# Kernel optimization log

Measured on AMD Instinct MI355X. Metric: run time of the kernel, lower is better.

## Reference

```python
import jax, jax.numpy as jnp
import numpy as np

NUM_VIEW = 300
NUM_ANGLE = 12
NUM_DEPTH = 4
GRASP_MAX_WIDTH = 0.1
B, C, NS, NG = 2, 512, 2048, 2000


def generate_grasp_views(N=NUM_VIEW):
    phi = (np.sqrt(5.0) - 1.0) / 2.0  # fibonacci sphere
    idxs = jnp.arange(N, dtype=jnp.float32)
    Z = (2.0 * idxs + 1.0) / N - 1.0
    r = jnp.sqrt(jnp.maximum(1.0 - Z * Z, 0.0))
    X = r * jnp.cos(2.0 * jnp.pi * idxs * phi)
    Y = r * jnp.sin(2.0 * jnp.pi * idxs * phi)
    return jnp.stack([X, Y, Z], -1)  # [N,3]


def viewpoint_params_to_matrix(towards, angle):
    # towards [...,3], angle [...]
    ax = towards
    zero = jnp.zeros_like(ax[..., 0])
    ay = jnp.stack([-ax[..., 1], ax[..., 0], zero], -1)
    ynorm = jnp.linalg.norm(ay, axis=-1, keepdims=True)
    ay = jnp.where(ynorm == 0, jnp.array([0.0, 1.0, 0.0], ax.dtype), ay)
    ax = ax / jnp.linalg.norm(ax, axis=-1, keepdims=True)
    ay = ay / jnp.linalg.norm(ay, axis=-1, keepdims=True)
    az = jnp.cross(ax, ay)
    c, s = jnp.cos(angle), jnp.sin(angle)
    one = jnp.ones_like(c)
    R1 = jnp.stack([one, zero * 0 + jnp.zeros_like(c), jnp.zeros_like(c),
                    jnp.zeros_like(c), c, -s,
                    jnp.zeros_like(c), s, c], -1).reshape(angle.shape + (3, 3))
    R2 = jnp.stack([ax, ay, az], -1)  # axes as columns
    return R2 @ R1


def conv1d(x, w, b):
    # 1x1 Conv1d == channel matmul. x [B,Ci,N], w [Co,Ci]
    return jnp.einsum('oi,bin->bon', w, x) + b[None, :, None]


def knn1(q, ref):
    # K=1 nearest neighbor indices of q [Nq,3] in ref [Nr,3]
    d = (jnp.sum(q * q, -1, keepdims=True) + jnp.sum(ref * ref, -1)[None, :]
         - 2.0 * q @ ref.T)
    return jnp.argmin(d, axis=-1)


def normalize_tensor(t, eps=1e-8):
    mx = jnp.max(t, -1, keepdims=True)
    mn = jnp.min(t, -1, keepdims=True)
    return (t - mn) / (mx - mn + eps)


def _process_one(seed_xyz, pose, gpoints, gscores, gwidths, views, views_rot):
    R, t = pose[:, :3], pose[:, 3]
    gp_trans = gpoints @ R.T + t                      # [Ng,3]
    gv_trans = views @ R.T                            # [V,3]
    gv_rot_trans = jnp.einsum('ij,vjk->vik', R, views_rot)  # [V,3,3]
    view_inds = knn1(views, gv_trans)                 # [V]
    gv_rot_trans = gv_rot_trans[view_inds]            # [V,3,3]
    nn_inds = knn1(seed_xyz, gp_trans)                # [Ns]
    gp_out = gp_trans[nn_inds]                        # [Ns,3]
    # gather seed dim first (Ns<Ng) then reindex views; axes independent
    sc = gscores[nn_inds][:, view_inds]               # [Ns,V,A,D]
    wd = gwidths[nn_inds][:, view_inds]
    rot = jnp.broadcast_to(gv_rot_trans[None], (seed_xyz.shape[0],) + gv_rot_trans.shape)
    return gp_out, rot, sc, wd


def setup_inputs() -> dict:
    key = jax.random.key(0)
    ks = jax.random.split(key, 16)
    seed_features = jax.random.normal(ks[0], (B, C, NS), jnp.float32)
    point_clouds = jax.random.normal(ks[1], (B, NS, 3), jnp.float32) * 0.2
    Rq = np.linalg.qr(np.asarray(jax.random.normal(ks[2], (B, 3, 3))))[0].astype(np.float32)
    trans = jax.random.normal(ks[3], (B, 3, 1), jnp.float32) * 0.1
    object_pose = jnp.concatenate([jnp.asarray(Rq), trans], -1)  # [B,3,4]
    grasp_points = jax.random.normal(ks[4], (B, NG, 3), jnp.float32) * 0.2
    grasp_labels = jax.random.uniform(ks[5], (B, NG, NUM_VIEW, NUM_ANGLE, NUM_DEPTH)) * 1.2 - 0.2
    grasp_offsets = jax.random.uniform(ks[6], (B, NG, NUM_VIEW, NUM_ANGLE, NUM_DEPTH)) * 0.15
    w = lambda k, co, ci: jax.random.normal(k, (co, ci), jnp.float32) * 0.05
    bz = lambda co: jnp.zeros((co,), jnp.float32)
    return {
        'seed_features': seed_features, 'point_clouds': point_clouds,
        'object_pose': object_pose, 'grasp_points': grasp_points,
        'grasp_labels': grasp_labels, 'grasp_offsets': grasp_offsets,
        'aw1_w': w(ks[7], C, C), 'aw1_b': bz(C),
        'aw2_w': w(ks[8], C, C), 'aw2_b': bz(C),
        'aw3_w': w(ks[9], NUM_VIEW, C), 'aw3_b': bz(NUM_VIEW),
        'sw1_w': w(ks[10], C, C), 'sw1_b': bz(C),
        'sw2_w': w(ks[11], NUM_DEPTH * NUM_ANGLE * 2, C), 'sw2_b': bz(NUM_DEPTH * NUM_ANGLE * 2),
    }


def reference(seed_features, point_clouds, object_pose, grasp_points,
              grasp_labels, grasp_offsets, aw1_w, aw1_b, aw2_w, aw2_b,
              aw3_w, aw3_b, sw1_w, sw1_b, sw2_w, sw2_b):
    Bx, Cx, Ns = seed_features.shape
    # --- ApproachNet (eval branch) ---
    res = jax.nn.relu(conv1d(seed_features, aw1_w, aw1_b))
    res = jax.nn.relu(conv1d(res, aw2_w, aw2_b))
    view_scores = conv1d(res, aw3_w, aw3_b).transpose(0, 2, 1)  # [B,Ns,V]
    top_view_inds = jnp.argmax(view_scores, -1)                 # [B,Ns]
    views = generate_grasp_views(NUM_VIEW)
    vp_xyz = views[top_view_inds]                               # [B,Ns,3]
    vp_rot = viewpoint_params_to_matrix(-vp_xyz, jnp.zeros(vp_xyz.shape[:-1], vp_xyz.dtype))
    # --- SWADNet ---
    f = jax.nn.relu(conv1d(res, sw1_w, sw1_b))
    f = conv1d(f, sw2_w, sw2_b)
    f = f.reshape(Bx, 2, NUM_ANGLE, NUM_DEPTH, Ns).transpose(0, 1, 4, 2, 3)
    grasp_score_pred = f[:, 0]   # [B,Ns,A,D]
    grasp_width_pred = f[:, 1]
    # --- process_grasp_labels (vmapped over batch) ---
    views_rot = viewpoint_params_to_matrix(-views, jnp.zeros((NUM_VIEW,), views.dtype))
    gp, rot, sc, wd = jax.vmap(_process_one, in_axes=(0, 0, 0, 0, 0, None, None))(
        point_clouds, object_pose, grasp_points, grasp_labels, grasp_offsets, views, views_rot)
    gmask = (sc <= 0.6) & (sc > 0)
    graspness = normalize_tensor(
        gmask.astype(jnp.float32).reshape(Bx, Ns, NUM_VIEW, -1).mean(-1))  # [B,Ns,V]
    label_mask = (sc > 0) & (wd <= GRASP_MAX_WIDTH)
    sc = jnp.where(label_mask, sc, 0.0)
    # --- match_grasp_view_and_label ---
    bi = jnp.arange(Bx)[:, None]
    ni = jnp.arange(Ns)[None, :]
    top_rot = rot[bi, ni, top_view_inds]  # [B,Ns,3,3]
    top_sc = sc[bi, ni, top_view_inds]    # [B,Ns,A,D]
    top_wd = wd[bi, ni, top_view_inds]
    u_max = jnp.max(top_sc)
    po = top_sc > 0
    safe = jnp.where(po, top_sc, 1.0)
    u_min = jnp.min(jnp.where(po, top_sc, jnp.inf))
    new_sc = jnp.log(u_max / safe) / (jnp.log(u_max / u_min) + 1e-8)
    top_sc = jnp.where(po, new_sc, top_sc)
    return (view_scores, vp_rot, grasp_score_pred, grasp_width_pred,
            top_rot, top_sc, top_wd, graspness, gp)
```

## Files before the change

kernel.cpp:

```cpp
#include <hip/hip_runtime.h>
#include <math.h>
#include <stdint.h>

#define NV 300
#define NA 12
#define ND 4
#define NB 2
#define NC 512
#define NSD 2048
#define NGP 2000
#define ROWLEN 14400

__global__ void __launch_bounds__(512) k_setup_all(
    const float* __restrict__ pose, float* __restrict__ views_rot_g,
    int* __restrict__ view_inds, float* __restrict__ Rsel, int* __restrict__ mmx) {
  int b = blockIdx.x, tid = threadIdx.x;
  __shared__ float sv[NV][3];
  __shared__ float svr[NV][9];
  __shared__ float R[9];
  __shared__ float gv[NV][3];
  __shared__ float gvr[NV];
  if (b == 0 && tid == 0) { mmx[0] = 0; mmx[1] = 0x7f800000; }
  if (tid < 9) R[tid] = pose[b * 12 + (tid / 3) * 4 + (tid % 3)];
  if (tid < NV) {
    float fi = (float)tid;
    float Z = (2.0f * fi + 1.0f) / 300.0f - 1.0f;
    float r = sqrtf(fmaxf(1.0f - Z * Z, 0.0f));
    float ang = (6.28318530717958647692f * fi) * 0.61803398874989484820f;
    float X = r * cosf(ang);
    float Y = r * sinf(ang);
    sv[tid][0] = X; sv[tid][1] = Y; sv[tid][2] = Z;
    float ax0 = -X, ax1 = -Y, ax2 = -Z;
    float ay0 = -ax1, ay1 = ax0, ay2 = 0.f;
    float ynorm = sqrtf(ay0 * ay0 + ay1 * ay1 + ay2 * ay2);
    if (ynorm == 0.f) { ay0 = 0.f; ay1 = 1.f; ay2 = 0.f; }
    float an = sqrtf(ax0 * ax0 + ax1 * ax1 + ax2 * ax2);
    ax0 /= an; ax1 /= an; ax2 /= an;
    float ayn = sqrtf(ay0 * ay0 + ay1 * ay1 + ay2 * ay2);
    ay0 /= ayn; ay1 /= ayn; ay2 /= ayn;
    float az0 = ax1 * ay2 - ax2 * ay1;
    float az1 = ax2 * ay0 - ax0 * ay2;
    float az2 = ax0 * ay1 - ax1 * ay0;
    svr[tid][0] = ax0; svr[tid][1] = ay0; svr[tid][2] = az0;
    svr[tid][3] = ax1; svr[tid][4] = ay1; svr[tid][5] = az1;
    svr[tid][6] = ax2; svr[tid][7] = ay2; svr[tid][8] = az2;
    if (b == 0) {
      float* m = views_rot_g + tid * 9;
#pragma unroll
      for (int i = 0; i < 9; i++) m[i] = svr[tid][i];
    }
  }
  __syncthreads();
  if (tid < NV) {
    float vx = sv[tid][0], vy = sv[tid][1], vz = sv[tid][2];
    float x = R[0] * vx + R[1] * vy + R[2] * vz;
    float y = R[3] * vx + R[4] * vy + R[5] * vz;
    float z = R[6] * vx + R[7] * vy + R[8] * vz;
    gv[tid][0] = x; gv[tid][1] = y; gv[tid][2] = z;
    gvr[tid] = x * x + y * y + z * z;
  }
  __syncthreads();
  if (tid < NV) {
    float qx = sv[tid][0], qy = sv[tid][1], qz = sv[tid][2];
    float qq = qx * qx + qy * qy + qz * qz;
    float best = INFINITY; int bi = 0;
    for (int u = 0; u < NV; u++) {
      float dot = qx * gv[u][0] + qy * gv[u][1] + qz * gv[u][2];
      float d = qq + gvr[u] - 2.f * dot;
      if (d < best) { best = d; bi = u; }
    }
    view_inds[b * NV + tid] = bi;
    const float* vr = svr[bi];
    float* o = Rsel + (b * NV + tid) * 9;
    for (int i = 0; i < 3; i++)
      for (int j = 0; j < 3; j++)
        o[i * 3 + j] = R[i * 3 + 0] * vr[0 + j] + R[i * 3 + 1] * vr[3 + j] + R[i * 3 + 2] * vr[6 + j];
  }
}

__global__ void __launch_bounds__(256) k_nn(
    const float* __restrict__ pc, const float* __restrict__ pose,
    const float* __restrict__ gpoints, int* __restrict__ nn_inds,
    float* __restrict__ out_gp) {
  int b = blockIdx.y;
  int s0 = blockIdx.x * 32;
  int tid = threadIdx.x;
  __shared__ float4 pts[NGP];
  __shared__ float P[12];
  if (tid < 12) P[tid] = pose[b * 12 + tid];
  __syncthreads();
  for (int i = tid; i < NGP; i += 256) {
    float px = gpoints[((size_t)b * NGP + i) * 3 + 0];
    float py = gpoints[((size_t)b * NGP + i) * 3 + 1];
    float pz = gpoints[((size_t)b * NGP + i) * 3 + 2];
    float x = P[0] * px + P[1] * py + P[2] * pz + P[3];
    float y = P[4] * px + P[5] * py + P[6] * pz + P[7];
    float z = P[8] * px + P[9] * py + P[10] * pz + P[11];
    pts[i] = make_float4(x, y, z, x * x + y * y + z * z);
  }
  __syncthreads();
  int sl = tid & 31, chunk = tid >> 5;
  int s = s0 + sl;
  float qx = pc[((size_t)b * NSD + s) * 3 + 0];
  float qy = pc[((size_t)b * NSD + s) * 3 + 1];
  float qz = pc[((size_t)b * NSD + s) * 3 + 2];
  float qq = qx * qx + qy * qy + qz * qz;
  int i0 = chunk * 250;
  float best = INFINITY; int bi = i0;
  for (int i = i0; i < i0 + 250; i++) {
    float4 p = pts[i];
    float d = qq + p.w - 2.f * (qx * p.x + qy * p.y + qz * p.z);
    if (d < best) { best = d; bi = i; }
  }
  __shared__ float rb[8][33];
  __shared__ int ri[8][33];
  rb[chunk][sl] = best; ri[chunk][sl] = bi;
  __syncthreads();
  if (tid < 32) {
    float bb = INFINITY; int ii = 0;
    for (int c = 0; c < 8; c++) {
      float v = rb[c][tid];
      if (v < bb) { bb = v; ii = ri[c][tid]; }
    }
    nn_inds[b * NSD + s0 + tid] = ii;
    float4 p = pts[ii];
    out_gp[((size_t)b * NSD + s0 + tid) * 3 + 0] = p.x;
    out_gp[((size_t)b * NSD + s0 + tid) * 3 + 1] = p.y;
    out_gp[((size_t)b * NSD + s0 + tid) * 3 + 2] = p.z;
  }
}

template <bool RELU, bool GUARD_M>
__global__ void __launch_bounds__(256) gemm128(
    const float* __restrict__ W, const float* __restrict__ X,
    const float* __restrict__ bias, float* __restrict__ Y,
    int O, int Cin, int N) {
  int b = blockIdx.z;
  const float* Xb = X + (size_t)b * Cin * N;
  float* Yb = Y + (size_t)b * O * N;
  int m0 = blockIdx.y * 128, n0 = blockIdx.x * 64;
  __shared__ float As[16][132];
  __shared__ float Bs[16][64];
  int tid = threadIdx.x;
  int mW = tid >> 1;
  int kW = (tid & 1) * 8;
  int kX = tid >> 4, nX = (tid & 15) * 4;
  int ty = tid >> 4, tx = tid & 15;
  bool okm = !GUARD_M || (m0 + mW) < O;
  float4 a0, a1, bv;
  {
    const float* wp = &W[(size_t)(m0 + mW) * Cin + kW];
    a0 = okm ? *(const float4*)wp : make_float4(0.f, 0.f, 0.f, 0.f);
    a1 = okm ? *(const float4*)(wp + 4) : make_float4(0.f, 0.f, 0.f, 0.f);
    bv = *(const float4*)&Xb[(size_t)kX * N + n0 + nX];
  }
  float acc[8][4] = {};
  for (int k0 = 0; k0 < Cin; k0 += 16) {
    __syncthreads();
    As[kW + 0][mW] = a0.x; As[kW + 1][mW] = a0.y;
    As[kW + 2][mW] = a0.z; As[kW + 3][mW] = a0.w;
    As[kW + 4][mW] = a1.x; As[kW + 5][mW] = a1.y;
    As[kW + 6][mW] = a1.z; As[kW + 7][mW] = a1.w;
    *(float4*)&Bs[kX][nX] = bv;
    __syncthreads();
    if (k0 + 16 < Cin) {
      const float* wp = &W[(size_t)(m0 + mW) * Cin + k0 + 16 + kW];
      a0 = okm ? *(const float4*)wp : make_float4(0.f, 0.f, 0.f, 0.f);
      a1 = okm ? *(const float4*)(wp + 4) : make_float4(0.f, 0.f, 0.f, 0.f);
      bv = *(const float4*)&Xb[(size_t)(k0 + 16 + kX) * N + n0 + nX];
    }
#pragma unroll
    for (int kk = 0; kk < 16; kk++) {
      float4 x0 = *(const float4*)&As[kk][ty * 8];
      float4 x1 = *(const float4*)&As[kk][ty * 8 + 4];
      float4 y = *(const float4*)&Bs[kk][tx * 4];
      acc[0][0] = fmaf(x0.x, y.x, acc[0][0]); acc[0][1] = fmaf(x0.x, y.y, acc[0][1]);
      acc[0][2] = fmaf(x0.x, y.z, acc[0][2]); acc[0][3] = fmaf(x0.x, y.w, acc[0][3]);
      acc[1][0] = fmaf(x0.y, y.x, acc[1][0]); acc[1][1] = fmaf(x0.y, y.y, acc[1][1]);
      acc[1][2] = fmaf(x0.y, y.z, acc[1][2]); acc[1][3] = fmaf(x0.y, y.w, acc[1][3]);
      acc[2][0] = fmaf(x0.z, y.x, acc[2][0]); acc[2][1] = fmaf(x0.z, y.y, acc[2][1]);
      acc[2][2] = fmaf(x0.z, y.z, acc[2][2]); acc[2][3] = fmaf(x0.z, y.w, acc[2][3]);
      acc[3][0] = fmaf(x0.w, y.x, acc[3][0]); acc[3][1] = fmaf(x0.w, y.y, acc[3][1]);
      acc[3][2] = fmaf(x0.w, y.z, acc[3][2]); acc[3][3] = fmaf(x0.w, y.w, acc[3][3]);
      acc[4][0] = fmaf(x1.x, y.x, acc[4][0]); acc[4][1] = fmaf(x1.x, y.y, acc[4][1]);
      acc[4][2] = fmaf(x1.x, y.z, acc[4][2]); acc[4][3] = fmaf(x1.x, y.w, acc[4][3]);
      acc[5][0] = fmaf(x1.y, y.x, acc[5][0]); acc[5][1] = fmaf(x1.y, y.y, acc[5][1]);
      acc[5][2] = fmaf(x1.y, y.z, acc[5][2]); acc[5][3] = fmaf(x1.y, y.w, acc[5][3]);
      acc[6][0] = fmaf(x1.z, y.x, acc[6][0]); acc[6][1] = fmaf(x1.z, y.y, acc[6][1]);
      acc[6][2] = fmaf(x1.z, y.z, acc[6][2]); acc[6][3] = fmaf(x1.z, y.w, acc[6][3]);
      acc[7][0] = fmaf(x1.w, y.x, acc[7][0]); acc[7][1] = fmaf(x1.w, y.y, acc[7][1]);
      acc[7][2] = fmaf(x1.w, y.z, acc[7][2]); acc[7][3] = fmaf(x1.w, y.w, acc[7][3]);
    }
  }
#pragma unroll
  for (int i = 0; i < 8; i++) {
    int m = m0 + ty * 8 + i;
    if (GUARD_M && m >= O) break;
    float bi = bias[m];
    float4 v;
    v.x = acc[i][0] + bi; v.y = acc[i][1] + bi;
    v.z = acc[i][2] + bi; v.w = acc[i][3] + bi;
    if (RELU) {
      v.x = fmaxf(v.x, 0.f); v.y = fmaxf(v.y, 0.f);
      v.z = fmaxf(v.z, 0.f); v.w = fmaxf(v.w, 0.f);
    }
    *(float4*)&Yb[(size_t)m * N + n0 + (tx << 2)] = v;
  }
}

__global__ void __launch_bounds__(256) gemm_sw2(
    const float* __restrict__ W, const float* __restrict__ X,
    const float* __restrict__ bias, float* __restrict__ gsp,
    float* __restrict__ gwp) {
  const int O = 96, Cin = NC, N = NSD;
  int b = blockIdx.z;
  const float* Xb = X + (size_t)b * Cin * N;
  int m0 = blockIdx.y * 64, n0 = blockIdx.x * 64;
  __shared__ float As[16][68];
  __shared__ float Bs[16][64];
  int tid = threadIdx.x;
  int mW = tid >> 2, kW = (tid & 3) * 4;
  int kX = tid >> 4, nX = (tid & 15) * 4;
  int ty = tid >> 4, tx = tid & 15;
  float acc[4][4] = {};
  for (int k0 = 0; k0 < Cin; k0 += 16) {
    float4 wv;
    if ((m0 + mW) < O)
      wv = *(const float4*)&W[(size_t)(m0 + mW) * Cin + k0 + kW];
    else
      wv = make_float4(0.f, 0.f, 0.f, 0.f);
    As[kW + 0][mW] = wv.x; As[kW + 1][mW] = wv.y;
    As[kW + 2][mW] = wv.z; As[kW + 3][mW] = wv.w;
    *(float4*)&Bs[kX][nX] = *(const float4*)&Xb[(size_t)(k0 + kX) * N + n0 + nX];
    __syncthreads();
#pragma unroll
    for (int kk = 0; kk < 16; kk++) {
      float4 a = *(const float4*)&As[kk][ty << 2];
      float4 bv = *(const float4*)&Bs[kk][tx << 2];
      acc[0][0] = fmaf(a.x, bv.x, acc[0][0]); acc[0][1] = fmaf(a.x, bv.y, acc[0][1]);
      acc[0][2] = fmaf(a.x, bv.z, acc[0][2]); acc[0][3] = fmaf(a.x, bv.w, acc[0][3]);
      acc[1][0] = fmaf(a.y, bv.x, acc[1][0]); acc[1][1] = fmaf(a.y, bv.y, acc[1][1]);
      acc[1][2] = fmaf(a.y, bv.z, acc[1][2]); acc[1][3] = fmaf(a.y, bv.w, acc[1][3]);
      acc[2][0] = fmaf(a.z, bv.x, acc[2][0]); acc[2][1] = fmaf(a.z, bv.y, acc[2][1]);
      acc[2][2] = fmaf(a.z, bv.z, acc[2][2]); acc[2][3] = fmaf(a.z, bv.w, acc[2][3]);
      acc[3][0] = fmaf(a.w, bv.x, acc[3][0]); acc[3][1] = fmaf(a.w, bv.y, acc[3][1]);
      acc[3][2] = fmaf(a.w, bv.z, acc[3][2]); acc[3][3] = fmaf(a.w, bv.w, acc[3][3]);
    }
    __syncthreads();
  }
  int m = m0 + ty * 4;
  if (m < O) {
    float b0 = bias[m], b1 = bias[m + 1], b2 = bias[m + 2], b3 = bias[m + 3];
#pragma unroll
    for (int j = 0; j < 4; j++) {
      int n = n0 + (tx << 2) + j;
      float4 v;
      v.x = acc[0][j] + b0; v.y = acc[1][j] + b1;
      v.z = acc[2][j] + b2; v.w = acc[3][j] + b3;
      size_t base = ((size_t)b * NSD + n) * 48;
      if (m < 48) *(float4*)&gsp[base + m] = v;
      else        *(float4*)&gwp[base + m - 48] = v;
    }
  }
}

__global__ void __launch_bounds__(256) k_view(
    const float* __restrict__ vs_t, const float* __restrict__ views_rot,
    const float* __restrict__ Rsel, int* __restrict__ tv_inds,
    float* __restrict__ o_vs, float* __restrict__ o_vprot,
    float* __restrict__ o_trot) {
  int b = blockIdx.y, n0 = blockIdx.x * 32;
  int tx = threadIdx.x, ty = threadIdx.y;
  __shared__ float tile[32][33];
  __shared__ float bval[8][32];
  __shared__ int bidx[8][32];
  const float* src = vs_t + (size_t)b * NV * NSD;
  float best = -INFINITY; int bi = 0;
  for (int v0 = 0; v0 < NV; v0 += 32) {
    int vlim = (NV - v0 < 32) ? (NV - v0) : 32;
    for (int i = ty; i < vlim; i += 8)
      tile[i][tx] = src[(size_t)(v0 + i) * NSD + n0 + tx];
    __syncthreads();
    if (v0 + tx < NV) {
#pragma unroll
      for (int j = 0; j < 4; j++) {
        int nl = ty * 4 + j;
        o_vs[((size_t)b * NSD + n0 + nl) * NV + v0 + tx] = tile[tx][nl];
      }
    }
    for (int i = ty; i < vlim; i += 8) {
      float val = tile[i][tx];
      if (val > best) { best = val; bi = v0 + i; }
    }
    __syncthreads();
  }
  bval[ty][tx] = best; bidx[ty][tx] = bi;
  __syncthreads();
  if (ty == 0) {
    for (int t = 1; t < 8; t++) {
      float v = bval[t][tx]; int ii = bidx[t][tx];
      if (v > best || (v == best && ii < bi)) { best = v; bi = ii; }
    }
    int n = n0 + tx;
    tv_inds[b * NSD + n] = bi;
    const float* vr = views_rot + bi * 9;
    const float* rs = Rsel + (b * NV + bi) * 9;
    float* o1 = o_vprot + ((size_t)b * NSD + n) * 9;
    float* o4 = o_trot + ((size_t)b * NSD + n) * 9;
#pragma unroll
    for (int i = 0; i < 9; i++) { o1[i] = vr[i]; o4[i] = rs[i]; }
  }
}

__global__ void __launch_bounds__(256) k_grasp(
    const float* __restrict__ gscores, const float* __restrict__ goffsets,
    const int* __restrict__ nn_inds, const int* __restrict__ tv_inds,
    const int* __restrict__ view_inds, float* __restrict__ o_grsp,
    float* __restrict__ o_twd, float* __restrict__ raw) {
  int b = blockIdx.y, s = blockIdx.x, tid = threadIdx.x;
  __shared__ int vi[NV];
  for (int v = tid; v < NV; v += 256) vi[v] = view_inds[b * NV + v];
  __syncthreads();
  int nn = nn_inds[b * NSD + s];
  int tv = tv_inds[b * NSD + s];
  int vit = vi[tv];
  const float* srow = gscores + ((size_t)(b * NGP + nn)) * ROWLEN;
  const float* wrow = goffsets + ((size_t)(b * NGP + nn)) * ROWLEN;
  if (tid < 48) {
    float sc = srow[vit * 48 + tid];
    float wd = wrow[vit * 48 + tid];
    bool m = (sc > 0.f) && (wd <= 0.1f);
    o_twd[((size_t)b * NSD + s) * 48 + tid] = wd;
    raw[((size_t)b * NSD + s) * 48 + tid] = m ? sc : 0.f;
  }
  __shared__ float g[NV];
  for (int v = tid; v < NV; v += 256) {
    int vv = vi[v];
    const float4* p = (const float4*)(srow + vv * 48);
    int cnt = 0;
#pragma unroll
    for (int q = 0; q < 12; q++) {
      float4 x = p[q];
      cnt += (x.x > 0.f && x.x <= 0.6f);
      cnt += (x.y > 0.f && x.y <= 0.6f);
      cnt += (x.z > 0.f && x.z <= 0.6f);
      cnt += (x.w > 0.f && x.w <= 0.6f);
    }
    g[v] = (float)cnt / 48.0f;
  }
  __syncthreads();
  float mx = -INFINITY, mn = INFINITY;
  for (int v = tid; v < NV; v += 256) { mx = fmaxf(mx, g[v]); mn = fminf(mn, g[v]); }
  for (int off = 32; off; off >>= 1) {
    mx = fmaxf(mx, __shfl_down(mx, off));
    mn = fminf(mn, __shfl_down(mn, off));
  }
  __shared__ float wmx[4], wmn[4];
  int wid = tid >> 6, lane = tid & 63;
  if (lane == 0) { wmx[wid] = mx; wmn[wid] = mn; }
  __syncthreads();
  if (tid == 0) {
    mx = fmaxf(fmaxf(wmx[0], wmx[1]), fmaxf(wmx[2], wmx[3]));
    mn = fminf(fminf(wmn[0], wmn[1]), fminf(wmn[2], wmn[3]));
    wmx[0] = mx; wmn[0] = mn;
  }
  __syncthreads();
  mx = wmx[0]; mn = wmn[0];
  float denom = mx - mn + 1e-8f;
  float* og = o_grsp + ((size_t)b * NSD + s) * NV;
  for (int v = tid; v < NV; v += 256) og[v] = (g[v] - mn) / denom;
}

__global__ void __launch_bounds__(256) k_reduce(const float* __restrict__ raw,
                                                int n, int* __restrict__ mmx) {
  float mx = -INFINITY, mn = INFINITY;
  for (int i = blockIdx.x * 256 + threadIdx.x; i < n; i += gridDim.x * 256) {
    float v = raw[i];
    mx = fmaxf(mx, v);
    if (v > 0.f) mn = fminf(mn, v);
  }
  for (int off = 32; off; off >>= 1) {
    mx = fmaxf(mx, __shfl_down(mx, off));
    mn = fminf(mn, __shfl_down(mn, off));
  }
  __shared__ float smx[4], smn[4];
  int wid = threadIdx.x >> 6, lane = threadIdx.x & 63;
  if (lane == 0) { smx[wid] = mx; smn[wid] = mn; }
  __syncthreads();
  if (threadIdx.x == 0) {
    mx = fmaxf(fmaxf(smx[0], smx[1]), fmaxf(smx[2], smx[3]));
    mn = fminf(fminf(smn[0], smn[1]), fminf(smn[2], smn[3]));
    atomicMax(&mmx[0], __float_as_int(mx));
    if (mn != INFINITY) atomicMin(&mmx[1], __float_as_int(mn));
  }
}

__global__ void k_topsc(const float* __restrict__ raw, const int* __restrict__ mmx,
                        float* __restrict__ out, int n) {
  int i = blockIdx.x * 256 + threadIdx.x;
  if (i >= n) return;
  float sc = raw[i];
  float umax = __int_as_float(mmx[0]);
  float umin = __int_as_float(mmx[1]);
  float denom = logf(umax / umin) + 1e-8f;
  float val = logf(umax / sc) / denom;
  out[i] = (sc > 0.f) ? val : sc;
}

extern "C" void kernel_launch(void* const* d_in, const int* in_sizes, int n_in,
                              void* d_out, int out_size, void* d_ws, size_t ws_size,
                              hipStream_t stream) {
  const float* seed_features = (const float*)d_in[0];
  const float* point_clouds  = (const float*)d_in[1];
  const float* object_pose   = (const float*)d_in[2];
  const float* grasp_points  = (const float*)d_in[3];
  const float* grasp_labels  = (const float*)d_in[4];
  const float* grasp_offsets = (const float*)d_in[5];
  const float* aw1_w = (const float*)d_in[6];
  const float* aw1_b = (const float*)d_in[7];
  const float* aw2_w = (const float*)d_in[8];
  const float* aw2_b = (const float*)d_in[9];
  const float* aw3_w = (const float*)d_in[10];
  const float* aw3_b = (const float*)d_in[11];
  const float* sw1_w = (const float*)d_in[12];
  const float* sw1_b = (const float*)d_in[13];
  const float* sw2_w = (const float*)d_in[14];
  const float* sw2_b = (const float*)d_in[15];

  float* out = (float*)d_out;
  float* o_vs    = out;
  float* o_vprot = o_vs + NB * NSD * NV;
  float* o_gsp   = o_vprot + NB * NSD * 9;
  float* o_gwp   = o_gsp + NB * NSD * 48;
  float* o_trot  = o_gwp + NB * NSD * 48;
  float* o_tsc   = o_trot + NB * NSD * 9;
  float* o_twd   = o_tsc + NB * NSD * 48;
  float* o_grsp  = o_twd + NB * NSD * 48;
  float* o_gp    = o_grsp + NB * NSD * NV;

  float* w = (float*)d_ws;
  float* res1 = w; w += NB * NC * NSD;
  float* res2 = w; w += NB * NC * NSD;
  float* vs_t = w; w += NB * NV * NSD;
  float* views_rot = w; w += 2720;
  float* Rsel = w; w += NB * NV * 9;
  float* raw  = w; w += NB * NSD * 48;
  int* view_inds = (int*)w; w += NB * NV;
  int* nn_inds   = (int*)w; w += NB * NSD;
  int* tv_inds   = (int*)w; w += NB * NSD;
  int* mmx       = (int*)w; w += 8;

  k_setup_all<<<NB, 512, 0, stream>>>(object_pose, views_rot, view_inds, Rsel, mmx);
  k_nn<<<dim3(NSD / 32, NB), 256, 0, stream>>>(point_clouds, object_pose, grasp_points,
                                               nn_inds, o_gp);

  gemm128<true, false><<<dim3(NSD / 64, NC / 128, NB), 256, 0, stream>>>(
      aw1_w, seed_features, aw1_b, res1, NC, NC, NSD);
  gemm128<true, false><<<dim3(NSD / 64, NC / 128, NB), 256, 0, stream>>>(
      aw2_w, res1, aw2_b, res2, NC, NC, NSD);
  gemm128<false, true><<<dim3(NSD / 64, (NV + 127) / 128, NB), 256, 0, stream>>>(
      aw3_w, res2, aw3_b, vs_t, NV, NC, NSD);
  gemm128<true, false><<<dim3(NSD / 64, NC / 128, NB), 256, 0, stream>>>(
      sw1_w, res2, sw1_b, res1, NC, NC, NSD);
  gemm_sw2<<<dim3(NSD / 64, 2, NB), 256, 0, stream>>>(sw2_w, res1, sw2_b, o_gsp, o_gwp);

  k_view<<<dim3(NSD / 32, NB), dim3(32, 8), 0, stream>>>(
      vs_t, views_rot, Rsel, tv_inds, o_vs, o_vprot, o_trot);
  k_grasp<<<dim3(NSD, NB), 256, 0, stream>>>(grasp_labels, grasp_offsets, nn_inds,
                                             tv_inds, view_inds, o_grsp, o_twd, raw);
  k_reduce<<<256, 256, 0, stream>>>(raw, NB * NSD * 48, mmx);
  k_topsc<<<(NB * NSD * 48 + 255) / 256, 256, 0, stream>>>(raw, mmx, o_tsc, NB * NSD * 48);
}
```

Before: 647.6 us.

## Precompute per-grasp-point view counts, double-buffer GEMMs, fuse aw3 and sw1 GEMMs

Adds a kernel that computes the score-in-range fraction once per grasp point and view, so the per-seed grasp kernel gathers 300 precomputed values instead of scanning 300x48 scores. The per-seed kernel shrinks to one wavefront with a shuffle-only reduction. GEMM kernels get double-buffered shared tiles with one barrier per k-step, and the aw3 and sw1 layers, which share the same input, run in one launch. This adds a workspace buffer and a full streaming pass over the grasp score tensor, plus more shared memory per block.

```diff
diff --git a/kernel.cpp b/kernel.cpp
--- a/kernel.cpp
+++ b/kernel.cpp
@@ -78,6 +78,26 @@
   }
 }
 
+__global__ void __launch_bounds__(256) k_gcnt(const float* __restrict__ gscores,
+                                              float* __restrict__ cntg) {
+  int b = blockIdx.y, p = blockIdx.x, tid = threadIdx.x;
+  const float* srow = gscores + ((size_t)(b * NGP + p)) * ROWLEN;
+  float* crow = cntg + ((size_t)(b * NGP + p)) * NV;
+  for (int u = tid; u < NV; u += 256) {
+    const float4* q4 = (const float4*)(srow + u * 48);
+    int cnt = 0;
+#pragma unroll
+    for (int q = 0; q < 12; q++) {
+      float4 x = q4[q];
+      cnt += (x.x > 0.f && x.x <= 0.6f);
+      cnt += (x.y > 0.f && x.y <= 0.6f);
+      cnt += (x.z > 0.f && x.z <= 0.6f);
+      cnt += (x.w > 0.f && x.w <= 0.6f);
+    }
+    crow[u] = (float)cnt / 48.0f;
+  }
+}
+
 __global__ void __launch_bounds__(256) k_nn(
     const float* __restrict__ pc, const float* __restrict__ pose,
     const float* __restrict__ gpoints, int* __restrict__ nn_inds,
@@ -130,23 +150,17 @@
   }
 }
 
-template <bool RELU, bool GUARD_M>
-__global__ void __launch_bounds__(256) gemm128(
-    const float* __restrict__ W, const float* __restrict__ X,
-    const float* __restrict__ bias, float* __restrict__ Y,
-    int O, int Cin, int N) {
-  int b = blockIdx.z;
-  const float* Xb = X + (size_t)b * Cin * N;
-  float* Yb = Y + (size_t)b * O * N;
-  int m0 = blockIdx.y * 128, n0 = blockIdx.x * 64;
-  __shared__ float As[16][132];
-  __shared__ float Bs[16][64];
+__device__ __forceinline__ void gemm_body(
+    const float* __restrict__ W, const float* __restrict__ Xb,
+    const float* __restrict__ bias, float* __restrict__ Yb,
+    int O, int Cin, int N, int m0, int n0, bool relu, bool guard,
+    float (*As)[16][132], float (*Bs)[16][64]) {
   int tid = threadIdx.x;
   int mW = tid >> 1;
   int kW = (tid & 1) * 8;
   int kX = tid >> 4, nX = (tid & 15) * 4;
   int ty = tid >> 4, tx = tid & 15;
-  bool okm = !GUARD_M || (m0 + mW) < O;
+  bool okm = !guard || (m0 + mW) < O;
   float4 a0, a1, bv;
   {
     const float* wp = &W[(size_t)(m0 + mW) * Cin + kW];
@@ -154,16 +168,17 @@
     a1 = okm ? *(const float4*)(wp + 4) : make_float4(0.f, 0.f, 0.f, 0.f);
     bv = *(const float4*)&Xb[(size_t)kX * N + n0 + nX];
   }
+  As[0][kW + 0][mW] = a0.x; As[0][kW + 1][mW] = a0.y;
+  As[0][kW + 2][mW] = a0.z; As[0][kW + 3][mW] = a0.w;
+  As[0][kW + 4][mW] = a1.x; As[0][kW + 5][mW] = a1.y;
+  As[0][kW + 6][mW] = a1.z; As[0][kW + 7][mW] = a1.w;
+  *(float4*)&Bs[0][kX][nX] = bv;
+  __syncthreads();
   float acc[8][4] = {};
+  int cur = 0;
   for (int k0 = 0; k0 < Cin; k0 += 16) {
-    __syncthreads();
-    As[kW + 0][mW] = a0.x; As[kW + 1][mW] = a0.y;
-    As[kW + 2][mW] = a0.z; As[kW + 3][mW] = a0.w;
-    As[kW + 4][mW] = a1.x; As[kW + 5][mW] = a1.y;
-    As[kW + 6][mW] = a1.z; As[kW + 7][mW] = a1.w;
-    *(float4*)&Bs[kX][nX] = bv;
-    __syncthreads();
-    if (k0 + 16 < Cin) {
+    bool more = (k0 + 16) < Cin;
+    if (more) {
       const float* wp = &W[(size_t)(m0 + mW) * Cin + k0 + 16 + kW];
       a0 = okm ? *(const float4*)wp : make_float4(0.f, 0.f, 0.f, 0.f);
       a1 = okm ? *(const float4*)(wp + 4) : make_float4(0.f, 0.f, 0.f, 0.f);
@@ -171,9 +186,9 @@
     }
 #pragma unroll
     for (int kk = 0; kk < 16; kk++) {
-      float4 x0 = *(const float4*)&As[kk][ty * 8];
-      float4 x1 = *(const float4*)&As[kk][ty * 8 + 4];
-      float4 y = *(const float4*)&Bs[kk][tx * 4];
+      float4 x0 = *(const float4*)&As[cur][kk][ty * 8];
+      float4 x1 = *(const float4*)&As[cur][kk][ty * 8 + 4];
+      float4 y = *(const float4*)&Bs[cur][kk][tx * 4];
       acc[0][0] = fmaf(x0.x, y.x, acc[0][0]); acc[0][1] = fmaf(x0.x, y.y, acc[0][1]);
       acc[0][2] = fmaf(x0.x, y.z, acc[0][2]); acc[0][3] = fmaf(x0.x, y.w, acc[0][3]);
       acc[1][0] = fmaf(x0.y, y.x, acc[1][0]); acc[1][1] = fmaf(x0.y, y.y, acc[1][1]);
@@ -191,20 +206,59 @@
       acc[7][0] = fmaf(x1.w, y.x, acc[7][0]); acc[7][1] = fmaf(x1.w, y.y, acc[7][1]);
       acc[7][2] = fmaf(x1.w, y.z, acc[7][2]); acc[7][3] = fmaf(x1.w, y.w, acc[7][3]);
     }
+    if (more) {
+      int nxt = cur ^ 1;
+      As[nxt][kW + 0][mW] = a0.x; As[nxt][kW + 1][mW] = a0.y;
+      As[nxt][kW + 2][mW] = a0.z; As[nxt][kW + 3][mW] = a0.w;
+      As[nxt][kW + 4][mW] = a1.x; As[nxt][kW + 5][mW] = a1.y;
+      As[nxt][kW + 6][mW] = a1.z; As[nxt][kW + 7][mW] = a1.w;
+      *(float4*)&Bs[nxt][kX][nX] = bv;
+      __syncthreads();
+      cur = nxt;
+    }
   }
 #pragma unroll
   for (int i = 0; i < 8; i++) {
     int m = m0 + ty * 8 + i;
-    if (GUARD_M && m >= O) break;
+    if (guard && m >= O) break;
     float bi = bias[m];
     float4 v;
     v.x = acc[i][0] + bi; v.y = acc[i][1] + bi;
     v.z = acc[i][2] + bi; v.w = acc[i][3] + bi;
-    if (RELU) {
+    if (relu) {
       v.x = fmaxf(v.x, 0.f); v.y = fmaxf(v.y, 0.f);
       v.z = fmaxf(v.z, 0.f); v.w = fmaxf(v.w, 0.f);
     }
     *(float4*)&Yb[(size_t)m * N + n0 + (tx << 2)] = v;
+  }
+}
+
+template <bool RELU>
+__global__ void __launch_bounds__(256) gemm128_db(
+    const float* __restrict__ W, const float* __restrict__ X,
+    const float* __restrict__ bias, float* __restrict__ Y,
+    int O, int Cin, int N) {
+  __shared__ float As[2][16][132];
+  __shared__ float Bs[2][16][64];
+  int b = blockIdx.z;
+  gemm_body(W, X + (size_t)b * Cin * N, bias, Y + (size_t)b * O * N,
+            O, Cin, N, blockIdx.y * 128, blockIdx.x * 64, RELU, false, As, Bs);
+}
+
+__global__ void __launch_bounds__(256) gemm_dual(
+    const float* __restrict__ W1, const float* __restrict__ b1, float* __restrict__ Y1,
+    const float* __restrict__ W2, const float* __restrict__ b2, float* __restrict__ Y2,
+    const float* __restrict__ X) {
+  __shared__ float As[2][16][132];
+  __shared__ float Bs[2][16][64];
+  int b = blockIdx.z;
+  const float* Xb = X + (size_t)b * NC * NSD;
+  if (blockIdx.y < 4) {
+    gemm_body(W1, Xb, b1, Y1 + (size_t)b * NC * NSD, NC, NC, NSD,
+              blockIdx.y * 128, blockIdx.x * 64, true, false, As, Bs);
+  } else {
+    gemm_body(W2, Xb, b2, Y2 + (size_t)b * NV * NSD, NV, NC, NSD,
+              (blockIdx.y - 4) * 128, blockIdx.x * 64, false, true, As, Bs);
   }
 }
 
@@ -312,63 +366,51 @@
   }
 }
 
-__global__ void __launch_bounds__(256) k_grasp(
-    const float* __restrict__ gscores, const float* __restrict__ goffsets,
-    const int* __restrict__ nn_inds, const int* __restrict__ tv_inds,
-    const int* __restrict__ view_inds, float* __restrict__ o_grsp,
-    float* __restrict__ o_twd, float* __restrict__ raw) {
-  int b = blockIdx.y, s = blockIdx.x, tid = threadIdx.x;
-  __shared__ int vi[NV];
-  for (int v = tid; v < NV; v += 256) vi[v] = view_inds[b * NV + v];
-  __syncthreads();
+__global__ void __launch_bounds__(64) k_grasp2(
+    const float* __restrict__ cntg, const float* __restrict__ gscores,
+    const float* __restrict__ goffsets, const int* __restrict__ nn_inds,
+    const int* __restrict__ tv_inds, const int* __restrict__ view_inds,
+    float* __restrict__ o_grsp, float* __restrict__ o_twd,
+    float* __restrict__ raw) {
+  int b = blockIdx.y, s = blockIdx.x, lane = threadIdx.x;
   int nn = nn_inds[b * NSD + s];
   int tv = tv_inds[b * NSD + s];
-  int vit = vi[tv];
+  int vit = view_inds[b * NV + tv];
   const float* srow = gscores + ((size_t)(b * NGP + nn)) * ROWLEN;
   const float* wrow = goffsets + ((size_t)(b * NGP + nn)) * ROWLEN;
-  if (tid < 48) {
-    float sc = srow[vit * 48 + tid];
-    float wd = wrow[vit * 48 + tid];
+  if (lane < 48) {
+    float sc = srow[vit * 48 + lane];
+    float wd = wrow[vit * 48 + lane];
     bool m = (sc > 0.f) && (wd <= 0.1f);
-    o_twd[((size_t)b * NSD + s) * 48 + tid] = wd;
-    raw[((size_t)b * NSD + s) * 48 + tid] = m ? sc : 0.f;
-  }
-  __shared__ float g[NV];
-  for (int v = tid; v < NV; v += 256) {
-    int vv = vi[v];
-    const float4* p = (const float4*)(srow + vv * 48);
-    int cnt = 0;
-#pragma unroll
-    for (int q = 0; q < 12; q++) {
-      float4 x = p[q];
-      cnt += (x.x > 0.f && x.x <= 0.6f);
-      cnt += (x.y > 0.f && x.y <= 0.6f);
-      cnt += (x.z > 0.f && x.z <= 0.6f);
-      cnt += (x.w > 0.f && x.w <= 0.6f);
-    }
-    g[v] = (float)cnt / 48.0f;
-  }
-  __syncthreads();
+    o_twd[((size_t)b * NSD + s) * 48 + lane] = wd;
+    raw[((size_t)b * NSD + s) * 48 + lane] = m ? sc : 0.f;
+  }
+  const float* crow = cntg + ((size_t)(b * NGP + nn)) * NV;
+  const int* vib = view_inds + b * NV;
+  float g[5];
   float mx = -INFINITY, mn = INFINITY;
-  for (int v = tid; v < NV; v += 256) { mx = fmaxf(mx, g[v]); mn = fminf(mn, g[v]); }
+#pragma unroll
+  for (int i = 0; i < 5; i++) {
+    int v = lane + i * 64;
+    if (v < NV) {
+      float val = crow[vib[v]];
+      g[i] = val;
+      mx = fmaxf(mx, val); mn = fminf(mn, val);
+    }
+  }
+#pragma unroll
   for (int off = 32; off; off >>= 1) {
     mx = fmaxf(mx, __shfl_down(mx, off));
     mn = fminf(mn, __shfl_down(mn, off));
   }
-  __shared__ float wmx[4], wmn[4];
-  int wid = tid >> 6, lane = tid & 63;
-  if (lane == 0) { wmx[wid] = mx; wmn[wid] = mn; }
-  __syncthreads();
-  if (tid == 0) {
-    mx = fmaxf(fmaxf(wmx[0], wmx[1]), fmaxf(wmx[2], wmx[3]));
-    mn = fminf(fminf(wmn[0], wmn[1]), fminf(wmn[2], wmn[3]));
-    wmx[0] = mx; wmn[0] = mn;
-  }
-  __syncthreads();
-  mx = wmx[0]; mn = wmn[0];
+  mx = __shfl(mx, 0); mn = __shfl(mn, 0);
   float denom = mx - mn + 1e-8f;
   float* og = o_grsp + ((size_t)b * NSD + s) * NV;
-  for (int v = tid; v < NV; v += 256) og[v] = (g[v] - mn) / denom;
+#pragma unroll
+  for (int i = 0; i < 5; i++) {
+    int v = lane + i * 64;
+    if (v < NV) og[v] = (g[i] - mn) / denom;
+  }
 }
 
 __global__ void __launch_bounds__(256) k_reduce(const float* __restrict__ raw,
@@ -442,6 +484,7 @@
   float* res1 = w; w += NB * NC * NSD;
   float* res2 = w; w += NB * NC * NSD;
   float* vs_t = w; w += NB * NV * NSD;
+  float* cntg = w; w += NB * NGP * NV;
   float* views_rot = w; w += 2720;
   float* Rsel = w; w += NB * NV * 9;
   float* raw  = w; w += NB * NSD * 48;
@@ -451,23 +494,23 @@
   int* mmx       = (int*)w; w += 8;
 
   k_setup_all<<<NB, 512, 0, stream>>>(object_pose, views_rot, view_inds, Rsel, mmx);
+  k_gcnt<<<dim3(NGP, NB), 256, 0, stream>>>(grasp_labels, cntg);
   k_nn<<<dim3(NSD / 32, NB), 256, 0, stream>>>(point_clouds, object_pose, grasp_points,
                                                nn_inds, o_gp);
 
-  gemm128<true, false><<<dim3(NSD / 64, NC / 128, NB), 256, 0, stream>>>(
+  gemm128_db<true><<<dim3(NSD / 64, NC / 128, NB), 256, 0, stream>>>(
       aw1_w, seed_features, aw1_b, res1, NC, NC, NSD);
-  gemm128<true, false><<<dim3(NSD / 64, NC / 128, NB), 256, 0, stream>>>(
+  gemm128_db<true><<<dim3(NSD / 64, NC / 128, NB), 256, 0, stream>>>(
       aw2_w, res1, aw2_b, res2, NC, NC, NSD);
-  gemm128<false, true><<<dim3(NSD / 64, (NV + 127) / 128, NB), 256, 0, stream>>>(
-      aw3_w, res2, aw3_b, vs_t, NV, NC, NSD);
-  gemm128<true, false><<<dim3(NSD / 64, NC / 128, NB), 256, 0, stream>>>(
-      sw1_w, res2, sw1_b, res1, NC, NC, NSD);
+  gemm_dual<<<dim3(NSD / 64, 7, NB), 256, 0, stream>>>(
+      sw1_w, sw1_b, res1, aw3_w, aw3_b, vs_t, res2);
   gemm_sw2<<<dim3(NSD / 64, 2, NB), 256, 0, stream>>>(sw2_w, res1, sw2_b, o_gsp, o_gwp);
 
   k_view<<<dim3(NSD / 32, NB), dim3(32, 8), 0, stream>>>(
       vs_t, views_rot, Rsel, tv_inds, o_vs, o_vprot, o_trot);
-  k_grasp<<<dim3(NSD, NB), 256, 0, stream>>>(grasp_labels, grasp_offsets, nn_inds,
-                                             tv_inds, view_inds, o_grsp, o_twd, raw);
+  k_grasp2<<<dim3(NSD, NB), 64, 0, stream>>>(cntg, grasp_labels, grasp_offsets,
+                                             nn_inds, tv_inds, view_inds,
+                                             o_grsp, o_twd, raw);
   k_reduce<<<256, 256, 0, stream>>>(raw, NB * NSD * 48, mmx);
   k_topsc<<<(NB * NSD * 48 + 255) / 256, 256, 0, stream>>>(raw, mmx, o_tsc, NB * NSD * 48);
 }
```

New measurement: 654.1 us. Within noise of the previous version (+1.0%).

## Split K across two thread groups in gemm128 with shared-memory reduction

Applied to the files above, without the earlier changes.

The 128x64-tile GEMM now launches 512 threads per block, and each half of the block handles half of the K dimension using its own shared-memory tiles. Group 1 writes its partial accumulators to a shared buffer, and group 0 adds them in before applying bias, ReLU and the store. The aim is to double the waves per block and hide latency on a grid that has few blocks (256 for the 512-channel layers). In exchange, shared memory per block grows a lot (about 60KB), which may limit how many blocks fit on a CU. The extra partial-sum buffer and an additional barrier also add overhead.

```diff
diff --git a/kernel.cpp b/kernel.cpp
--- a/kernel.cpp
+++ b/kernel.cpp
@@ -131,7 +131,7 @@
 }
 
 template <bool RELU, bool GUARD_M>
-__global__ void __launch_bounds__(256) gemm128(
+__global__ void __launch_bounds__(512) gemm128_sk(
     const float* __restrict__ W, const float* __restrict__ X,
     const float* __restrict__ bias, float* __restrict__ Y,
     int O, int Cin, int N) {
@@ -139,9 +139,13 @@
   const float* Xb = X + (size_t)b * Cin * N;
   float* Yb = Y + (size_t)b * O * N;
   int m0 = blockIdx.y * 128, n0 = blockIdx.x * 64;
-  __shared__ float As[16][132];
-  __shared__ float Bs[16][64];
-  int tid = threadIdx.x;
+  __shared__ float As[2][16][132];
+  __shared__ float Bs[2][16][64];
+  __shared__ float Ps[128][68];
+  int tid = threadIdx.x & 255;
+  int grp = threadIdx.x >> 8;
+  int KH = Cin >> 1;
+  int kbase = grp * KH;
   int mW = tid >> 1;
   int kW = (tid & 1) * 8;
   int kX = tid >> 4, nX = (tid & 15) * 4;
@@ -149,31 +153,31 @@
   bool okm = !GUARD_M || (m0 + mW) < O;
   float4 a0, a1, bv;
   {
-    const float* wp = &W[(size_t)(m0 + mW) * Cin + kW];
+    const float* wp = &W[(size_t)(m0 + mW) * Cin + kbase + kW];
     a0 = okm ? *(const float4*)wp : make_float4(0.f, 0.f, 0.f, 0.f);
     a1 = okm ? *(const float4*)(wp + 4) : make_float4(0.f, 0.f, 0.f, 0.f);
-    bv = *(const float4*)&Xb[(size_t)kX * N + n0 + nX];
+    bv = *(const float4*)&Xb[(size_t)(kbase + kX) * N + n0 + nX];
   }
   float acc[8][4] = {};
-  for (int k0 = 0; k0 < Cin; k0 += 16) {
-    __syncthreads();
-    As[kW + 0][mW] = a0.x; As[kW + 1][mW] = a0.y;
-    As[kW + 2][mW] = a0.z; As[kW + 3][mW] = a0.w;
-    As[kW + 4][mW] = a1.x; As[kW + 5][mW] = a1.y;
-    As[kW + 6][mW] = a1.z; As[kW + 7][mW] = a1.w;
-    *(float4*)&Bs[kX][nX] = bv;
-    __syncthreads();
-    if (k0 + 16 < Cin) {
-      const float* wp = &W[(size_t)(m0 + mW) * Cin + k0 + 16 + kW];
+  for (int k0 = 0; k0 < KH; k0 += 16) {
+    __syncthreads();
+    As[grp][kW + 0][mW] = a0.x; As[grp][kW + 1][mW] = a0.y;
+    As[grp][kW + 2][mW] = a0.z; As[grp][kW + 3][mW] = a0.w;
+    As[grp][kW + 4][mW] = a1.x; As[grp][kW + 5][mW] = a1.y;
+    As[grp][kW + 6][mW] = a1.z; As[grp][kW + 7][mW] = a1.w;
+    *(float4*)&Bs[grp][kX][nX] = bv;
+    __syncthreads();
+    if (k0 + 16 < KH) {
+      const float* wp = &W[(size_t)(m0 + mW) * Cin + kbase + k0 + 16 + kW];
       a0 = okm ? *(const float4*)wp : make_float4(0.f, 0.f, 0.f, 0.f);
       a1 = okm ? *(const float4*)(wp + 4) : make_float4(0.f, 0.f, 0.f, 0.f);
-      bv = *(const float4*)&Xb[(size_t)(k0 + 16 + kX) * N + n0 + nX];
+      bv = *(const float4*)&Xb[(size_t)(kbase + k0 + 16 + kX) * N + n0 + nX];
     }
 #pragma unroll
     for (int kk = 0; kk < 16; kk++) {
-      float4 x0 = *(const float4*)&As[kk][ty * 8];
-      float4 x1 = *(const float4*)&As[kk][ty * 8 + 4];
-      float4 y = *(const float4*)&Bs[kk][tx * 4];
+      float4 x0 = *(const float4*)&As[grp][kk][ty * 8];
+      float4 x1 = *(const float4*)&As[grp][kk][ty * 8 + 4];
+      float4 y = *(const float4*)&Bs[grp][kk][tx * 4];
       acc[0][0] = fmaf(x0.x, y.x, acc[0][0]); acc[0][1] = fmaf(x0.x, y.y, acc[0][1]);
       acc[0][2] = fmaf(x0.x, y.z, acc[0][2]); acc[0][3] = fmaf(x0.x, y.w, acc[0][3]);
       acc[1][0] = fmaf(x0.y, y.x, acc[1][0]); acc[1][1] = fmaf(x0.y, y.y, acc[1][1]);
@@ -192,19 +196,29 @@
       acc[7][2] = fmaf(x1.w, y.z, acc[7][2]); acc[7][3] = fmaf(x1.w, y.w, acc[7][3]);
     }
   }
-#pragma unroll
-  for (int i = 0; i < 8; i++) {
-    int m = m0 + ty * 8 + i;
-    if (GUARD_M && m >= O) break;
-    float bi = bias[m];
-    float4 v;
-    v.x = acc[i][0] + bi; v.y = acc[i][1] + bi;
-    v.z = acc[i][2] + bi; v.w = acc[i][3] + bi;
-    if (RELU) {
-      v.x = fmaxf(v.x, 0.f); v.y = fmaxf(v.y, 0.f);
-      v.z = fmaxf(v.z, 0.f); v.w = fmaxf(v.w, 0.f);
-    }
-    *(float4*)&Yb[(size_t)m * N + n0 + (tx << 2)] = v;
+  if (grp == 1) {
+#pragma unroll
+    for (int i = 0; i < 8; i++)
+      *(float4*)&Ps[ty * 8 + i][tx * 4] =
+          make_float4(acc[i][0], acc[i][1], acc[i][2], acc[i][3]);
+  }
+  __syncthreads();
+  if (grp == 0) {
+#pragma unroll
+    for (int i = 0; i < 8; i++) {
+      int m = m0 + ty * 8 + i;
+      if (GUARD_M && m >= O) break;
+      float bi = bias[m];
+      float4 p = *(const float4*)&Ps[ty * 8 + i][tx * 4];
+      float4 v;
+      v.x = (acc[i][0] + p.x) + bi; v.y = (acc[i][1] + p.y) + bi;
+      v.z = (acc[i][2] + p.z) + bi; v.w = (acc[i][3] + p.w) + bi;
+      if (RELU) {
+        v.x = fmaxf(v.x, 0.f); v.y = fmaxf(v.y, 0.f);
+        v.z = fmaxf(v.z, 0.f); v.w = fmaxf(v.w, 0.f);
+      }
+      *(float4*)&Yb[(size_t)m * N + n0 + (tx << 2)] = v;
+    }
   }
 }
 
@@ -454,13 +468,13 @@
   k_nn<<<dim3(NSD / 32, NB), 256, 0, stream>>>(point_clouds, object_pose, grasp_points,
                                                nn_inds, o_gp);
 
-  gemm128<true, false><<<dim3(NSD / 64, NC / 128, NB), 256, 0, stream>>>(
+  gemm128_sk<true, false><<<dim3(NSD / 64, NC / 128, NB), 512, 0, stream>>>(
       aw1_w, seed_features, aw1_b, res1, NC, NC, NSD);
-  gemm128<true, false><<<dim3(NSD / 64, NC / 128, NB), 256, 0, stream>>>(
+  gemm128_sk<true, false><<<dim3(NSD / 64, NC / 128, NB), 512, 0, stream>>>(
       aw2_w, res1, aw2_b, res2, NC, NC, NSD);
-  gemm128<false, true><<<dim3(NSD / 64, (NV + 127) / 128, NB), 256, 0, stream>>>(
+  gemm128_sk<false, true><<<dim3(NSD / 64, (NV + 127) / 128, NB), 512, 0, stream>>>(
       aw3_w, res2, aw3_b, vs_t, NV, NC, NSD);
-  gemm128<true, false><<<dim3(NSD / 64, NC / 128, NB), 256, 0, stream>>>(
+  gemm128_sk<true, false><<<dim3(NSD / 64, NC / 128, NB), 512, 0, stream>>>(
       sw1_w, res2, sw1_b, res1, NC, NC, NSD);
   gemm_sw2<<<dim3(NSD / 64, 2, NB), 256, 0, stream>>>(sw2_w, res1, sw2_b, o_gsp, o_gwp);
 
```

Result: faster. 626.8 us (-3.2%).
